# Optimization experiments

Hardware: AMD Instinct MI355X
Metric: run time of the kernel (lower is better)

Reference implementation:

```python
import jax, jax.numpy as jnp
import numpy as np

B, L = 128, 200
NUM_C, D, M = 10000, 128, 64


def setup_inputs() -> dict:
    key = jax.random.key(0)
    ks = jax.random.split(key, 16)
    n = lambda k, s, sc=0.05: jax.random.normal(k, s, dtype=jnp.float32) * sc
    return {
        "q": jax.random.randint(ks[0], (B, L), 0, NUM_C),
        "r": jax.random.randint(ks[1], (B, L), 0, 2),
        "k_emb": n(ks[2], (NUM_C, D)),
        "v_emb": n(ks[3], (2, D)),
        "Mk": n(ks[4], (M, D), 0.2),   # kaiming_normal_
        "Mv0": n(ks[5], (M, D), 0.2),  # kaiming_normal_
        "f_W": n(ks[6], (D, 2 * D)), "f_b": jnp.zeros((D,), jnp.float32),
        "e_W": n(ks[7], (D, D)), "e_b": jnp.zeros((D,), jnp.float32),
        "a_W": n(ks[8], (D, D)), "a_b": jnp.zeros((D,), jnp.float32),
        "ab_W": n(ks[9], (1, D)), "ab_b": jnp.zeros((1,), jnp.float32),
        "df_W": n(ks[10], (1, D)), "df_b": jnp.zeros((1,), jnp.float32),
    }


def reference(q, r, k_emb, v_emb, Mk, Mv0, f_W, f_b, e_W, e_b, a_W, a_b, ab_W, ab_b, df_W, df_b):
    # Embeddings
    k = k_emb[q]                # [B, L, D] question key embedding
    v = k + v_emb[r]            # [B, L, D] value embedding

    # Attention over memory slots, erase/add gates
    w = jax.nn.softmax(jnp.einsum('bld,md->blm', k, Mk), axis=-1)   # [B, L, M]
    e = jax.nn.sigmoid(jnp.einsum('bld,ed->ble', v, e_W) + e_b)      # erase [B, L, D]
    a = jnp.tanh(jnp.einsum('bld,ed->ble', v, a_W) + a_b)            # add   [B, L, D]

    Mvt0 = jnp.broadcast_to(Mv0[None], (q.shape[0], Mv0.shape[0], Mv0.shape[1]))  # [B, M, D]

    def step(Mvt, inp):
        wt, et, at = inp  # [B,M], [B,D], [B,D]
        # read uses memory BEFORE this timestep's write (Mv[:, :-1] in torch)
        read = jnp.einsum('bm,bmd->bd', wt, Mvt)
        we = wt[:, :, None]
        Mvt_new = Mvt * (1.0 - we * et[:, None, :]) + we * at[:, None, :]
        return Mvt_new, read

    _, reads = jax.lax.scan(
        step, Mvt0,
        (w.transpose(1, 0, 2), e.transpose(1, 0, 2), a.transpose(1, 0, 2)))
    reads = reads.transpose(1, 0, 2)  # [B, L, D]

    f = jnp.tanh(jnp.concatenate([reads, k], axis=-1) @ f_W.T + f_b)  # [B, L, D]
    stu_ability = jnp.tanh(f @ ab_W.T + ab_b)   # [B, L, 1] (dropout is identity in eval)
    que_diff = jnp.tanh(k @ df_W.T + df_b)      # [B, L, 1]
    p = jax.nn.sigmoid(3.0 * stu_ability - que_diff)
    return p.squeeze(-1)  # [B, L]
```

## Files before the change

### kernel.cpp

```cpp
#include <hip/hip_runtime.h>

typedef unsigned short ushort_t;
typedef short bf16x8 __attribute__((ext_vector_type(8)));
typedef float f32x4 __attribute__((ext_vector_type(4)));

#define B_ 128
#define L_ 200
#define D_ 128
#define M_ 64

__device__ __forceinline__ float fast_sigmoid(float x) {
    return 1.f / (1.f + __expf(-x));
}

__device__ __forceinline__ float fast_tanh(float x) {
    float xc = fminf(fmaxf(x, -15.f), 15.f);
    float e = __expf(2.f * xc);
    return (e - 1.f) / (e + 1.f);
}

__device__ __forceinline__ ushort_t f2bf(float f) {
    union { float f; unsigned int u; } x;
    x.f = f;
    unsigned int u = x.u;
    unsigned int r = (u + 0x7FFFu + ((u >> 16) & 1u)) >> 16;
    return (ushort_t)r;
}

__device__ __forceinline__ uint4 pack8(float4 a, float4 b) {
    uint4 u;
    u.x = (unsigned)f2bf(a.x) | ((unsigned)f2bf(a.y) << 16);
    u.y = (unsigned)f2bf(a.z) | ((unsigned)f2bf(a.w) << 16);
    u.z = (unsigned)f2bf(b.x) | ((unsigned)f2bf(b.y) << 16);
    u.w = (unsigned)f2bf(b.z) | ((unsigned)f2bf(b.w) << 16);
    return u;
}

#define F_WQ   0u
#define F_EAQ  1638400u
#define F_FKQ  8192000u
#define F_RD   11468800u
#define F_DIFF 14745600u
#define F_PACK 14771200u
#define WPACK_N 57344
#define FPACK_N 16384

__global__ __launch_bounds__(256) void k_pack(
    const float* __restrict__ Mk, const float* __restrict__ eW,
    const float* __restrict__ aW, const float* __restrict__ fW,
    ushort_t* __restrict__ Wpack, ushort_t* __restrict__ Fpack)
{
    int i = blockIdx.x * 256 + threadIdx.x;
    if (i < WPACK_N) {
        int g = i >> 9, lane = (i >> 3) & 63, j = i & 7;
        int nt = g >> 2, ks = g & 3;
        int col = nt * 16 + (lane & 15);
        int d = ks * 32 + ((lane >> 4) << 3) + j;
        float v;
        if (col < 64)       v = Mk[col * 128 + d];
        else if (col < 192) v = eW[(col - 64) * 128 + d];
        else if (col < 320) v = aW[(col - 192) * 128 + d];
        else                v = fW[(col - 320) * 256 + 128 + d];
        Wpack[i] = f2bf(v);
    } else if (i < WPACK_N + FPACK_N) {
        int e = i - WPACK_N;
        int g = e >> 9, lane = (e >> 3) & 63, j = e & 7;
        int nt = g >> 2, ks = g & 3;
        int col = nt * 16 + (lane & 15);
        int d = ks * 32 + ((lane >> 4) << 3) + j;
        Fpack[e] = f2bf(fW[col * 256 + d]);
    }
}

__device__ __forceinline__ void loadB4(const ushort_t* __restrict__ base,
                                       int nt, int lane, bf16x8* b) {
    const ushort_t* p = base + (nt * 256 + lane) * 8;
    b[0] = *(const bf16x8*)(p);
    b[1] = *(const bf16x8*)(p + 512);
    b[2] = *(const bf16x8*)(p + 1024);
    b[3] = *(const bf16x8*)(p + 1536);
}

__global__ __launch_bounds__(512) void k_pre_mfma(
    const int* __restrict__ q, const int* __restrict__ r,
    const float* __restrict__ k_emb, const float* __restrict__ v_emb,
    const ushort_t* __restrict__ Wpack,
    const float* __restrict__ e_b, const float* __restrict__ a_b,
    const float* __restrict__ df_W, const float* __restrict__ df_b,
    float* __restrict__ wq, float* __restrict__ eaq,
    float* __restrict__ fkq, float* __restrict__ diffq)
{
    __shared__ ushort_t skA[8192];
    __shared__ ushort_t svA[8192];
    __shared__ float slog[64 * 68];

    const int tid = threadIdx.x;
    const int pos0 = blockIdx.x * 64;
    const int wave = tid >> 6;
    const int lane = tid & 63;
    const int mt = wave & 3;
    const int nh = wave >> 2;

    #pragma unroll
    for (int i = 0; i < 2; i++) {
        int E = tid + 512 * i;
        int mtile = E >> 8, ks = (E >> 6) & 3, le = E & 63;
        int prow = pos0 + mtile * 16 + (le & 15);
        int dof = ks * 32 + ((le >> 4) << 3);
        int qv = q[prow], rv = r[prow];
        const float4* kp = (const float4*)(k_emb + qv * 128 + dof);
        float4 ka = kp[0], kb = kp[1];
        const float4* vp = (const float4*)(v_emb + rv * 128 + dof);
        float4 va = vp[0], vb = vp[1];
        *(uint4*)&skA[E * 8] = pack8(ka, kb);
        float4 s0, s1;
        s0.x = ka.x + va.x; s0.y = ka.y + va.y; s0.z = ka.z + va.z; s0.w = ka.w + va.w;
        s1.x = kb.x + vb.x; s1.y = kb.y + vb.y; s1.z = kb.z + vb.z; s1.w = kb.w + vb.w;
        *(uint4*)&svA[E * 8] = pack8(s0, s1);
    }
    __syncthreads();

    bf16x8 A[4];
    {
        const ushort_t* src = nh ? svA : skA;
        #pragma unroll
        for (int ks = 0; ks < 4; ks++)
            A[ks] = *(const bf16x8*)&src[((mt * 4 + ks) * 64 + lane) * 8];
    }

    const int col = lane & 15;
    const int quad = lane >> 4;
    const int rbase = mt * 16 + quad * 4;

    if (nh == 0) {
        bf16x8 Bb[2][4];
        loadB4(Wpack, 0, lane, Bb[0]);
        #pragma unroll
        for (int j = 0; j < 12; j++) {
            if (j < 11) {
                int jn = j + 1;
                loadB4(Wpack, (jn < 4) ? jn : jn + 16, lane, Bb[jn & 1]);
            }
            f32x4 acc = {0.f, 0.f, 0.f, 0.f};
            #pragma unroll
            for (int ks = 0; ks < 4; ks++)
                acc = __builtin_amdgcn_mfma_f32_16x16x32_bf16(A[ks], Bb[j & 1][ks], acc, 0, 0, 0);
            if (j < 4) {
                #pragma unroll
                for (int reg = 0; reg < 4; reg++)
                    slog[(rbase + reg) * 68 + j * 16 + col] = acc[reg];
            } else {
                int c = (j - 4) * 16 + col;
                #pragma unroll
                for (int reg = 0; reg < 4; reg++)
                    fkq[(pos0 + rbase + reg) * 128 + c] = acc[reg];
            }
        }
        {
            int row = tid >> 2, ln = tid & 3;
            const float* lr = slog + row * 68 + ln * 16;
            float v[16];
            #pragma unroll
            for (int j = 0; j < 16; j++) v[j] = lr[j];
            float mx = v[0];
            #pragma unroll
            for (int j = 1; j < 16; j++) mx = fmaxf(mx, v[j]);
            mx = fmaxf(mx, __shfl_xor(mx, 1));
            mx = fmaxf(mx, __shfl_xor(mx, 2));
            float s = 0.f;
            #pragma unroll
            for (int j = 0; j < 16; j++) { v[j] = __expf(v[j] - mx); s += v[j]; }
            s += __shfl_xor(s, 1); s += __shfl_xor(s, 2);
            float inv = 1.f / s;
            float* wout = wq + (pos0 + row) * 64 + ln * 16;
            #pragma unroll
            for (int j = 0; j < 16; j++) wout[j] = v[j] * inv;
        }
    } else {
        bf16x8 Be[2][4], Ba[2][4];
        loadB4(Wpack, 4, lane, Be[0]);
        loadB4(Wpack, 12, lane, Ba[0]);
        #pragma unroll
        for (int i = 0; i < 8; i++) {
            if (i < 7) {
                loadB4(Wpack, 5 + i, lane, Be[(i + 1) & 1]);
                loadB4(Wpack, 13 + i, lane, Ba[(i + 1) & 1]);
            }
            f32x4 ae = {0.f, 0.f, 0.f, 0.f};
            f32x4 aa = {0.f, 0.f, 0.f, 0.f};
            #pragma unroll
            for (int ks = 0; ks < 4; ks++) {
                ae = __builtin_amdgcn_mfma_f32_16x16x32_bf16(A[ks], Be[i & 1][ks], ae, 0, 0, 0);
                aa = __builtin_amdgcn_mfma_f32_16x16x32_bf16(A[ks], Ba[i & 1][ks], aa, 0, 0, 0);
            }
            int c = i * 16 + col;
            float ebv = e_b[c], abv = a_b[c];
            #pragma unroll
            for (int reg = 0; reg < 4; reg++) {
                float2 o;
                o.x = fast_sigmoid(ae[reg] + ebv);
                o.y = fast_tanh(aa[reg] + abv);
                *(float2*)(eaq + ((pos0 + rbase + reg) * 128 + c) * 2) = o;
            }
        }
        {
            int t2 = tid - 256;
            int row = t2 >> 2, ln = t2 & 3;
            int pos = pos0 + row;
            int qv = q[pos];
            const float4* kp = (const float4*)(k_emb + qv * 128) + ln * 8;
            const float4* dfp = (const float4*)df_W + ln * 8;
            float s = 0.f;
            #pragma unroll
            for (int j = 0; j < 8; j++) {
                float4 a = kp[j], b = dfp[j];
                s = fmaf(a.x, b.x, fmaf(a.y, b.y, fmaf(a.z, b.z, fmaf(a.w, b.w, s))));
            }
            s += __shfl_xor(s, 1); s += __shfl_xor(s, 2);
            if (ln == 0) diffq[pos] = fast_tanh(s + df_b[0]);
        }
    }
}

#define SC_PREFETCH(wX, eX, cN)                                            \
    _Pragma("unroll")                                                      \
    for (int tt = 0; tt < 8; tt++) {                                       \
        wX[2 * tt]     = wb4[((cN) * 8 + tt) * 16 + sc * 2];               \
        wX[2 * tt + 1] = wb4[((cN) * 8 + tt) * 16 + sc * 2 + 1];           \
        eX[tt]         = eab[((cN) * 8 + tt) * 128];                       \
    }

#define SC_COMPUTE(wX, eX, bb)                                             \
    _Pragma("unroll")                                                      \
    for (int tt = 0; tt < 8; tt++) {                                       \
        float4 u = wX[2 * tt], v = wX[2 * tt + 1];                         \
        float2 ea = eX[tt];                                                \
        float ev = ea.x, av = ea.y, ne = -ev;                              \
        float r0 = u.x * Mv[0];                                            \
        float r1 = u.y * Mv[1];                                            \
        r0 = fmaf(u.z, Mv[2], r0); r1 = fmaf(u.w, Mv[3], r1);              \
        r0 = fmaf(v.x, Mv[4], r0); r1 = fmaf(v.y, Mv[5], r1);              \
        r0 = fmaf(v.z, Mv[6], r0); r1 = fmaf(v.w, Mv[7], r1);              \
        Mv[0] = fmaf(u.x, fmaf(ne, Mv[0], av), Mv[0]);                     \
        Mv[1] = fmaf(u.y, fmaf(ne, Mv[1], av), Mv[1]);                     \
        Mv[2] = fmaf(u.z, fmaf(ne, Mv[2], av), Mv[2]);                     \
        Mv[3] = fmaf(u.w, fmaf(ne, Mv[3], av), Mv[3]);                     \
        Mv[4] = fmaf(v.x, fmaf(ne, Mv[4], av), Mv[4]);                     \
        Mv[5] = fmaf(v.y, fmaf(ne, Mv[5], av), Mv[5]);                     \
        Mv[6] = fmaf(v.z, fmaf(ne, Mv[6], av), Mv[6]);                     \
        Mv[7] = fmaf(v.w, fmaf(ne, Mv[7], av), Mv[7]);                     \
        pbuf[bb][sc][tt][lane] = r0 + r1;                                  \
    }

#define SC_REDUCE(bb, c0) {                                                \
        float s = pbuf[bb][0][wv][lane] + pbuf[bb][1][wv][lane]            \
                + pbuf[bb][2][wv][lane] + pbuf[bb][3][wv][lane]            \
                + pbuf[bb][4][wv][lane] + pbuf[bb][5][wv][lane]            \
                + pbuf[bb][6][wv][lane] + pbuf[bb][7][wv][lane];           \
        rbase[((c0) * 8 + wv) * 128 + lane] = s;                           \
    }

__global__ __launch_bounds__(512, 2) void k_scan(
    const float* __restrict__ wq, const float* __restrict__ eaq,
    const float* __restrict__ Mv0, float* __restrict__ reads)
{
    __shared__ float pbuf[2][8][8][64];

    const int tid = threadIdx.x;
    const int b = blockIdx.x >> 1;
    const int dh = blockIdx.x & 1;
    const int wv = tid >> 6;
    const int sc = __builtin_amdgcn_readfirstlane(wv);
    const int lane = tid & 63;
    const int d = dh * 64 + lane;

    float Mv[8];
    #pragma unroll
    for (int j = 0; j < 8; j++) Mv[j] = Mv0[(sc * 8 + j) * D_ + d];

    const float4* wb4 = (const float4*)(wq + b * (L_ * M_));
    const float2* eab = (const float2*)eaq + b * (L_ * 128) + d;
    float* rbase = reads + b * (L_ * D_) + dh * 64;

    float4 wA[16], wB[16];
    float2 eA[8], eB[8];

    SC_PREFETCH(wA, eA, 0);

    for (int cc = 0; cc < 12; cc++) {
        const int c0 = 2 * cc;
        SC_PREFETCH(wB, eB, c0 + 1);
        SC_COMPUTE(wA, eA, 0);
        __syncthreads();
        SC_REDUCE(0, c0);
        SC_PREFETCH(wA, eA, c0 + 2);
        SC_COMPUTE(wB, eB, 1);
        __syncthreads();
        SC_REDUCE(1, c0 + 1);
    }
    SC_COMPUTE(wA, eA, 0);
    __syncthreads();
    SC_REDUCE(0, 24);
}

__global__ __launch_bounds__(512) void k_final_mfma(
    const float* __restrict__ reads, const float* __restrict__ fkq,
    const float* __restrict__ diffq, const ushort_t* __restrict__ Fpack,
    const float* __restrict__ f_b, const float* __restrict__ ab_W,
    const float* __restrict__ ab_b, float* __restrict__ out)
{
    __shared__ ushort_t srA[8192];
    __shared__ float sab[64 * 2];

    const int tid = threadIdx.x;
    const int pos0 = blockIdx.x * 64;
    const int wave = tid >> 6;
    const int lane = tid & 63;
    const int mt = wave & 3;
    const int half = wave >> 2;

    #pragma unroll
    for (int i = 0; i < 2; i++) {
        int E = tid + 512 * i;
        int mtile = E >> 8, ks = (E >> 6) & 3, le = E & 63;
        int prow = pos0 + mtile * 16 + (le & 15);
        int dof = ks * 32 + ((le >> 4) << 3);
        const float4* rp = (const float4*)(reads + prow * 128 + dof);
        *(uint4*)&srA[E * 8] = pack8(rp[0], rp[1]);
    }

    const int col = lane & 15;
    const int quad = lane >> 4;
    const int rbase = mt * 16 + quad * 4;

    float fkv[16];
    #pragma unroll
    for (int i = 0; i < 4; i++)
        #pragma unroll
        for (int reg = 0; reg < 4; reg++)
            fkv[i * 4 + reg] = fkq[(pos0 + rbase + reg) * 128 + (half * 4 + i) * 16 + col];

    __syncthreads();

    bf16x8 A[4];
    #pragma unroll
    for (int ks = 0; ks < 4; ks++)
        A[ks] = *(const bf16x8*)&srA[((mt * 4 + ks) * 64 + lane) * 8];

    float abacc[4] = {0.f, 0.f, 0.f, 0.f};

    bf16x8 Bb[2][4];
    loadB4(Fpack, half * 4, lane, Bb[0]);
    #pragma unroll
    for (int i = 0; i < 4; i++) {
        if (i < 3) loadB4(Fpack, half * 4 + i + 1, lane, Bb[(i + 1) & 1]);
        f32x4 acc = {0.f, 0.f, 0.f, 0.f};
        #pragma unroll
        for (int ks = 0; ks < 4; ks++)
            acc = __builtin_amdgcn_mfma_f32_16x16x32_bf16(A[ks], Bb[i & 1][ks], acc, 0, 0, 0);
        int c = (half * 4 + i) * 16 + col;
        float fb = f_b[c];
        float abw = ab_W[c];
        #pragma unroll
        for (int reg = 0; reg < 4; reg++) {
            float fv = fast_tanh(acc[reg] + fkv[i * 4 + reg] + fb);
            abacc[reg] = fmaf(abw, fv, abacc[reg]);
        }
    }

    #pragma unroll
    for (int reg = 0; reg < 4; reg++) {
        float v = abacc[reg];
        v += __shfl_xor(v, 1); v += __shfl_xor(v, 2);
        v += __shfl_xor(v, 4); v += __shfl_xor(v, 8);
        abacc[reg] = v;
    }
    if (col == 0) {
        #pragma unroll
        for (int reg = 0; reg < 4; reg++)
            sab[(rbase + reg) * 2 + half] = abacc[reg];
    }
    __syncthreads();
    if (tid < 64) {
        float ab = fast_tanh(sab[tid * 2] + sab[tid * 2 + 1] + ab_b[0]);
        int pos = pos0 + tid;
        out[pos] = fast_sigmoid(3.f * ab - diffq[pos]);
    }
}

extern "C" void kernel_launch(void* const* d_in, const int* in_sizes, int n_in,
                              void* d_out, int out_size, void* d_ws, size_t ws_size,
                              hipStream_t stream)
{
    const int*   q     = (const int*)d_in[0];
    const int*   r     = (const int*)d_in[1];
    const float* k_emb = (const float*)d_in[2];
    const float* v_emb = (const float*)d_in[3];
    const float* Mk    = (const float*)d_in[4];
    const float* Mv0   = (const float*)d_in[5];
    const float* f_W   = (const float*)d_in[6];
    const float* f_b   = (const float*)d_in[7];
    const float* e_W   = (const float*)d_in[8];
    const float* e_b   = (const float*)d_in[9];
    const float* a_W   = (const float*)d_in[10];
    const float* a_b   = (const float*)d_in[11];
    const float* ab_W  = (const float*)d_in[12];
    const float* ab_b  = (const float*)d_in[13];
    const float* df_W  = (const float*)d_in[14];
    const float* df_b  = (const float*)d_in[15];

    float* ws = (float*)d_ws;
    float* out = (float*)d_out;
    ushort_t* Wpack = (ushort_t*)(ws + F_PACK);
    ushort_t* Fpack = Wpack + WPACK_N;

    k_pack<<<288, 256, 0, stream>>>(Mk, e_W, a_W, f_W, Wpack, Fpack);

    k_pre_mfma<<<400, 512, 0, stream>>>(
        q, r, k_emb, v_emb, Wpack, e_b, a_b, df_W, df_b,
        ws + F_WQ, ws + F_EAQ, ws + F_FKQ, ws + F_DIFF);

    k_scan<<<256, 512, 0, stream>>>(
        ws + F_WQ, ws + F_EAQ, Mv0, ws + F_RD);

    k_final_mfma<<<400, 512, 0, stream>>>(
        ws + F_RD, ws + F_FKQ, ws + F_DIFF, Fpack,
        f_b, ab_W, ab_b, out);
}
```

Before: 149.7 us.

## Store intermediate erase/add, fk and reads buffers in half precision

```diff
diff --git a/kernel.cpp b/kernel.cpp
--- a/kernel.cpp
+++ b/kernel.cpp
@@ -1,6 +1,7 @@
 #include <hip/hip_runtime.h>
 
 typedef unsigned short ushort_t;
+typedef _Float16 f16_t;
 typedef short bf16x8 __attribute__((ext_vector_type(8)));
 typedef float f32x4 __attribute__((ext_vector_type(4)));
 
@@ -34,6 +35,22 @@
     u.z = (unsigned)f2bf(b.x) | ((unsigned)f2bf(b.y) << 16);
     u.w = (unsigned)f2bf(b.z) | ((unsigned)f2bf(b.w) << 16);
     return u;
+}
+
+__device__ __forceinline__ unsigned pack_ea(float e, float a) {
+    union { f16_t h[2]; unsigned u; } p;
+    p.h[0] = (f16_t)e;
+    p.h[1] = (f16_t)a;
+    return p.u;
+}
+
+__device__ __forceinline__ float2 unpack_ea(unsigned u) {
+    union { unsigned u; f16_t h[2]; } p;
+    p.u = u;
+    float2 r;
+    r.x = (float)p.h[0];
+    r.y = (float)p.h[1];
+    return r;
 }
 
 #define F_WQ   0u
@@ -87,8 +104,8 @@
     const ushort_t* __restrict__ Wpack,
     const float* __restrict__ e_b, const float* __restrict__ a_b,
     const float* __restrict__ df_W, const float* __restrict__ df_b,
-    float* __restrict__ wq, float* __restrict__ eaq,
-    float* __restrict__ fkq, float* __restrict__ diffq)
+    float* __restrict__ wq, unsigned* __restrict__ eaq,
+    f16_t* __restrict__ fkq, float* __restrict__ diffq)
 {
     __shared__ ushort_t skA[8192];
     __shared__ ushort_t svA[8192];
@@ -153,7 +170,7 @@
                 int c = (j - 4) * 16 + col;
                 #pragma unroll
                 for (int reg = 0; reg < 4; reg++)
-                    fkq[(pos0 + rbase + reg) * 128 + c] = acc[reg];
+                    fkq[(pos0 + rbase + reg) * 128 + c] = (f16_t)acc[reg];
             }
         }
         {
@@ -174,7 +191,14 @@
             float inv = 1.f / s;
             float* wout = wq + (pos0 + row) * 64 + ln * 16;
             #pragma unroll
-            for (int j = 0; j < 16; j++) wout[j] = v[j] * inv;
+            for (int j4 = 0; j4 < 4; j4++) {
+                float4 o;
+                o.x = v[j4 * 4 + 0] * inv;
+                o.y = v[j4 * 4 + 1] * inv;
+                o.z = v[j4 * 4 + 2] * inv;
+                o.w = v[j4 * 4 + 3] * inv;
+                *(float4*)(wout + j4 * 4) = o;
+            }
         }
     } else {
         bf16x8 Be[2][4], Ba[2][4];
@@ -197,10 +221,9 @@
             float ebv = e_b[c], abv = a_b[c];
             #pragma unroll
             for (int reg = 0; reg < 4; reg++) {
-                float2 o;
-                o.x = fast_sigmoid(ae[reg] + ebv);
-                o.y = fast_tanh(aa[reg] + abv);
-                *(float2*)(eaq + ((pos0 + rbase + reg) * 128 + c) * 2) = o;
+                float ev = fast_sigmoid(ae[reg] + ebv);
+                float av = fast_tanh(aa[reg] + abv);
+                eaq[(pos0 + rbase + reg) * 128 + c] = pack_ea(ev, av);
             }
         }
         {
@@ -227,7 +250,7 @@
     for (int tt = 0; tt < 8; tt++) {                                       \
         wX[2 * tt]     = wb4[((cN) * 8 + tt) * 16 + sc * 2];               \
         wX[2 * tt + 1] = wb4[((cN) * 8 + tt) * 16 + sc * 2 + 1];           \
-        eX[tt]         = eab[((cN) * 8 + tt) * 128];                       \
+        eX[tt]         = unpack_ea(eab[((cN) * 8 + tt) * 128]);            \
     }
 
 #define SC_COMPUTE(wX, eX, bb)                                             \
@@ -257,12 +280,12 @@
                 + pbuf[bb][2][wv][lane] + pbuf[bb][3][wv][lane]            \
                 + pbuf[bb][4][wv][lane] + pbuf[bb][5][wv][lane]            \
                 + pbuf[bb][6][wv][lane] + pbuf[bb][7][wv][lane];           \
-        rbase[((c0) * 8 + wv) * 128 + lane] = s;                           \
+        rbase[((c0) * 8 + wv) * 128 + lane] = f2bf(s);                     \
     }
 
 __global__ __launch_bounds__(512, 2) void k_scan(
-    const float* __restrict__ wq, const float* __restrict__ eaq,
-    const float* __restrict__ Mv0, float* __restrict__ reads)
+    const float* __restrict__ wq, const unsigned* __restrict__ eaq,
+    const float* __restrict__ Mv0, ushort_t* __restrict__ reads)
 {
     __shared__ float pbuf[2][8][8][64];
 
@@ -279,8 +302,8 @@
     for (int j = 0; j < 8; j++) Mv[j] = Mv0[(sc * 8 + j) * D_ + d];
 
     const float4* wb4 = (const float4*)(wq + b * (L_ * M_));
-    const float2* eab = (const float2*)eaq + b * (L_ * 128) + d;
-    float* rbase = reads + b * (L_ * D_) + dh * 64;
+    const unsigned* eab = eaq + b * (L_ * 128) + d;
+    ushort_t* rbase = reads + b * (L_ * D_) + dh * 64;
 
     float4 wA[16], wB[16];
     float2 eA[8], eB[8];
@@ -304,7 +327,7 @@
 }
 
 __global__ __launch_bounds__(512) void k_final_mfma(
-    const float* __restrict__ reads, const float* __restrict__ fkq,
+    const ushort_t* __restrict__ reads, const f16_t* __restrict__ fkq,
     const float* __restrict__ diffq, const ushort_t* __restrict__ Fpack,
     const float* __restrict__ f_b, const float* __restrict__ ab_W,
     const float* __restrict__ ab_b, float* __restrict__ out)
@@ -325,8 +348,7 @@
         int mtile = E >> 8, ks = (E >> 6) & 3, le = E & 63;
         int prow = pos0 + mtile * 16 + (le & 15);
         int dof = ks * 32 + ((le >> 4) << 3);
-        const float4* rp = (const float4*)(reads + prow * 128 + dof);
-        *(uint4*)&srA[E * 8] = pack8(rp[0], rp[1]);
+        *(uint4*)&srA[E * 8] = *(const uint4*)(reads + prow * 128 + dof);
     }
 
     const int col = lane & 15;
@@ -338,7 +360,7 @@
     for (int i = 0; i < 4; i++)
         #pragma unroll
         for (int reg = 0; reg < 4; reg++)
-            fkv[i * 4 + reg] = fkq[(pos0 + rbase + reg) * 128 + (half * 4 + i) * 16 + col];
+            fkv[i * 4 + reg] = (float)fkq[(pos0 + rbase + reg) * 128 + (half * 4 + i) * 16 + col];
 
     __syncthreads();
 
@@ -411,6 +433,9 @@
 
     float* ws = (float*)d_ws;
     float* out = (float*)d_out;
+    unsigned* eaq_u   = (unsigned*)(ws + F_EAQ);
+    f16_t*    fkq_h   = (f16_t*)(ws + F_FKQ);
+    ushort_t* reads_b = (ushort_t*)(ws + F_RD);
     ushort_t* Wpack = (ushort_t*)(ws + F_PACK);
     ushort_t* Fpack = Wpack + WPACK_N;
 
@@ -418,12 +443,12 @@
 
     k_pre_mfma<<<400, 512, 0, stream>>>(
         q, r, k_emb, v_emb, Wpack, e_b, a_b, df_W, df_b,
-        ws + F_WQ, ws + F_EAQ, ws + F_FKQ, ws + F_DIFF);
+        ws + F_WQ, eaq_u, fkq_h, ws + F_DIFF);
 
     k_scan<<<256, 512, 0, stream>>>(
-        ws + F_WQ, ws + F_EAQ, Mv0, ws + F_RD);
+        ws + F_WQ, eaq_u, Mv0, reads_b);
 
     k_final_mfma<<<400, 512, 0, stream>>>(
-        ws + F_RD, ws + F_FKQ, ws + F_DIFF, Fpack,
+        reads_b, fkq_h, ws + F_DIFF, Fpack,
         f_b, ab_W, ab_b, out);
 }
```

Result: faster. 146.3 us (-2.3%).
